# Kernel tuning notes

Measured on AMD Instinct MI355X. Metric: run time of the kernel, lower is better.

## Reference

```python
import jax, jax.numpy as jnp
import numpy as np

NUM_BUCKETS = 32
MAX_DISTANCE = 128
N_HEADS = 16
D_KV = 64


def relative_position_bucket(rel, num_buckets=NUM_BUCKETS, max_distance=MAX_DISTANCE):
    # bidirectional (encoder) bucketing, matches the torch reference
    nb = num_buckets // 2
    ret = (rel > 0).astype(jnp.int32) * nb
    rp = jnp.abs(rel)
    max_exact = nb // 2
    is_small = rp < max_exact
    # guard log(0); masked out by is_small anyway
    large = max_exact + (
        jnp.log(jnp.maximum(rp, 1).astype(jnp.float32) / max_exact)
        / np.log(max_distance / max_exact)
        * (nb - max_exact)
    ).astype(jnp.int32)
    large = jnp.minimum(large, nb - 1)
    return ret + jnp.where(is_small, rp, large)


def compute_bias(rel_bias_table, q_len, k_len):
    q_pos = jnp.arange(q_len)[:, None]
    k_pos = jnp.arange(k_len)[None, :]
    buckets = relative_position_bucket(k_pos - q_pos)  # [S, K]
    bias = rel_bias_table[buckets]                      # [S, K, H]
    return jnp.transpose(bias, (2, 0, 1))[None]         # [1, H, S, K]


def setup_inputs() -> dict:
    key = jax.random.key(0)
    ks = jax.random.split(key, 6)
    d_model, inner = 1024, N_HEADS * D_KV
    scale = 1.0 / np.sqrt(d_model)
    return {
        "hidden_states": jax.random.normal(ks[0], (4, 2048, d_model), jnp.float32),
        "Wq": jax.random.normal(ks[1], (d_model, inner), jnp.float32) * scale,
        "Wk": jax.random.normal(ks[2], (d_model, inner), jnp.float32) * scale,
        "Wv": jax.random.normal(ks[3], (d_model, inner), jnp.float32) * scale,
        "Wo": jax.random.normal(ks[4], (inner, d_model), jnp.float32) * scale,
        "rel_bias_table": jax.random.normal(ks[5], (NUM_BUCKETS, N_HEADS), jnp.float32),
    }


def reference(hidden_states, Wq, Wk, Wv, Wo, rel_bias_table):
    B, S, _ = hidden_states.shape
    K_len = S  # self-attention (key_value_states is None)
    q = (hidden_states @ Wq).reshape(B, S, N_HEADS, D_KV)
    k = (hidden_states @ Wk).reshape(B, K_len, N_HEADS, D_KV)
    v = (hidden_states @ Wv).reshape(B, K_len, N_HEADS, D_KV)
    # NOTE: T5 attention has no 1/sqrt(d_kv) scaling
    scores = jnp.einsum("bshd,bkhd->bhsk", q, k)
    pos_bias = compute_bias(rel_bias_table, S, K_len)
    attn = jax.nn.softmax(scores + pos_bias, axis=-1)
    out = jnp.einsum("bhsk,bkhd->bshd", attn, v).reshape(B, S, N_HEADS * D_KV)
    out = out @ Wo
    return (out, pos_bias)
```

## Files before the change

### kernel.cpp

```cpp
#include <hip/hip_runtime.h>
#include <cstdint>
#include <cstddef>

typedef unsigned short u16;
typedef unsigned int u32;
typedef __attribute__((ext_vector_type(8))) short bf16x8;
typedef __attribute__((ext_vector_type(4))) float f32x4;
typedef __attribute__((ext_vector_type(16))) float f32x16;
typedef __attribute__((ext_vector_type(2))) unsigned int u32x2;

#define MFMA(a, b, c)   __builtin_amdgcn_mfma_f32_16x16x32_bf16((a), (b), (c), 0, 0, 0)
#define MFMA32(a, b, c) __builtin_amdgcn_mfma_f32_32x32x16_bf16((a), (b), (c), 0, 0, 0)

typedef const __attribute__((address_space(1))) void gv1_t;
typedef __attribute__((address_space(3))) void lv3_t;
#define GLOAD_LDS16(g, l) __builtin_amdgcn_global_load_lds((gv1_t*)(g), (lv3_t*)(l), 16, 0, 0)

#define BATCH 4
#define SEQ 2048
#define DMODEL 1024
#define NHEAD 16
#define MROWS (BATCH * SEQ)
#define QKVN (3 * DMODEL)

#define LOG2E 1.44269504088896340736f

__device__ __forceinline__ u16 f2bf(float f) {
  u32 x = __builtin_bit_cast(u32, f);
  x += 0x7fffu + ((x >> 16) & 1u);
  return (u16)(x >> 16);
}

__device__ __forceinline__ u32 pkbf(float a, float b) {
  return (u32)f2bf(a) | ((u32)f2bf(b) << 16);
}

__device__ __forceinline__ u32x2 plswap(u32 a, u32 b) {
  return __builtin_amdgcn_permlane32_swap(a, b, false, false);
}

extern "C" __device__ float __ocml_exp2_f32(float);
__device__ __forceinline__ float exp2fast(float x) {
#if __has_builtin(__builtin_amdgcn_exp2f)
  return __builtin_amdgcn_exp2f(x);
#else
  return __ocml_exp2_f32(x);
#endif
}

__global__ __launch_bounds__(256) void convert_h(const float* __restrict__ H,
                                                 u16* __restrict__ Hb) {
  size_t i = (size_t)blockIdx.x * 1024 + threadIdx.x * 4;
  float4 v = *(const float4*)&H[i];
  uint2 o;
  o.x = pkbf(v.x, v.y);
  o.y = pkbf(v.z, v.w);
  *(uint2*)&Hb[i] = o;
}

__global__ void transpose_w(const float* __restrict__ Wq, const float* __restrict__ Wk,
                            const float* __restrict__ Wv, const float* __restrict__ Wo,
                            u16* __restrict__ Wt) {
  __shared__ u16 Ts[32][33];
  const float* W = (blockIdx.z == 0) ? Wq : (blockIdx.z == 1) ? Wk
                   : (blockIdx.z == 2) ? Wv : Wo;
  const float s = (blockIdx.z == 0) ? LOG2E : 1.0f;
  int x = threadIdx.x, y0 = threadIdx.y;
  int r0 = blockIdx.y * 32, c0 = blockIdx.x * 32;
  for (int yy = y0; yy < 32; yy += 8)
    Ts[yy][x] = f2bf(W[(size_t)(r0 + yy) * 1024 + c0 + x] * s);
  __syncthreads();
  for (int yy = y0; yy < 32; yy += 8)
    Wt[(size_t)(blockIdx.z * 1024 + c0 + yy) * 1024 + r0 + x] = Ts[x][yy];
}

__device__ __forceinline__ int rel_bucket(int rel) {
  int ret = (rel > 0) ? 16 : 0;
  int rp = (rel < 0) ? -rel : rel;
  if (rp < 8) return ret + rp;
  int i = 0;
  i += (rp >= 12); i += (rp >= 16); i += (rp >= 23); i += (rp >= 32);
  i += (rp >= 46); i += (rp >= 64); i += (rp >= 91);
  return ret + 8 + i;
}

__global__ __launch_bounds__(256) void build_bias_rel(const float* __restrict__ tbl,
                                                      float* __restrict__ brel,
                                                      float* __restrict__ brel2) {
  int h = blockIdx.x;
  for (int rix = threadIdx.x; rix < 4095; rix += 256) {
    float v = tbl[rel_bucket(rix - 2047) * NHEAD + h];
    brel[h * 4096 + rix] = v;
    brel2[h * 4096 + rix] = v * LOG2E;
  }
}

__global__ __launch_bounds__(256) void gemm_bf16k(const u16* __restrict__ A,
                                                  const u16* __restrict__ Bt,
                                                  u16* __restrict__ Cb, float* __restrict__ Cf,
                                                  int M, int N, int K) {
  __shared__ u16 As[128 * 32];
  __shared__ u16 Bs[128 * 32];
  const int t = threadIdx.x;
  const int w = t >> 6, lane = t & 63, quad = lane >> 4, l15 = lane & 15;
  const int wr = w >> 1, wc = w & 1;

  const int nwg = gridDim.x * gridDim.y;
  const int orig = blockIdx.y * gridDim.x + blockIdx.x;
  const int wg = (orig & 7) * (nwg >> 3) + (orig >> 3);
  const int bx = wg % gridDim.x, by = wg / gridDim.x;
  const int row0 = by * 128, col0 = bx * 128;

  f32x4 acc[4][4];
  #pragma unroll
  for (int i = 0; i < 4; ++i)
    #pragma unroll
    for (int j = 0; j < 4; ++j) acc[i][j] = (f32x4){0.f, 0.f, 0.f, 0.f};

  const int srow = lane >> 2, scol = (lane & 3) * 8;

  for (int k0 = 0; k0 < K; k0 += 32) {
    #pragma unroll
    for (int p = 0; p < 2; ++p) {
      const int rb = w * 32 + p * 16;
      GLOAD_LDS16(&A[(size_t)(row0 + rb + srow) * K + k0 + scol], &As[rb * 32]);
      GLOAD_LDS16(&Bt[(size_t)(col0 + rb + srow) * K + k0 + scol], &Bs[rb * 32]);
    }
    __syncthreads();
    bf16x8 af[4], bfr[4];
    #pragma unroll
    for (int i = 0; i < 4; ++i)
      af[i] = *(const bf16x8*)&As[(wr * 64 + i * 16 + l15) * 32 + quad * 8];
    #pragma unroll
    for (int j = 0; j < 4; ++j)
      bfr[j] = *(const bf16x8*)&Bs[(wc * 64 + j * 16 + l15) * 32 + quad * 8];
    #pragma unroll
    for (int i = 0; i < 4; ++i)
      #pragma unroll
      for (int j = 0; j < 4; ++j)
        acc[i][j] = MFMA(af[i], bfr[j], acc[i][j]);
    __syncthreads();
  }
  #pragma unroll
  for (int i = 0; i < 4; ++i) {
    #pragma unroll
    for (int j = 0; j < 4; ++j) {
      int col = col0 + wc * 64 + j * 16 + l15;
      #pragma unroll
      for (int r = 0; r < 4; ++r) {
        int row = row0 + wr * 64 + i * 16 + quad * 4 + r;
        if (Cb) Cb[(size_t)row * N + col] = f2bf(acc[i][j][r]);
        else    Cf[(size_t)row * N + col] = acc[i][j][r];
      }
    }
  }
}

__global__ __launch_bounds__(256) void transpose_v(const u16* __restrict__ QKV,
                                                   u16* __restrict__ Vt) {
  __shared__ u16 Ts[64 * 72];
  int st = blockIdx.x, bh = blockIdx.y;
  int b = bh >> 4, h = bh & 15;
  int t = threadIdx.x;
  #pragma unroll
  for (int p = 0; p < 2; ++p) {
    int c = t * 2 + p, r = c >> 3, cc = (c & 7) * 8;
    *(uint4*)&Ts[r * 72 + cc] =
        *(const uint4*)&QKV[(size_t)(b * SEQ + st * 64 + r) * QKVN + 2 * DMODEL + h * 64 + cc];
  }
  __syncthreads();
  #pragma unroll
  for (int p = 0; p < 2; ++p) {
    int c = t * 2 + p, d = c >> 3, s8 = (c & 7) * 8;
    union { u16 u[8]; uint4 v; } tmp;
    #pragma unroll
    for (int jj = 0; jj < 8; ++jj) tmp.u[jj] = Ts[(s8 + jj) * 72 + d];
    *(uint4*)&Vt[((size_t)(bh * 64 + d)) * SEQ + st * 64 + s8] = tmp.v;
  }
}

__global__ __launch_bounds__(256) void attn_fused(const u16* __restrict__ QKV,
                                                  const u16* __restrict__ Vt,
                                                  const float* __restrict__ brel,
                                                  const float* __restrict__ brel2,
                                                  u16* __restrict__ Aout,
                                                  float* __restrict__ pb) {
  __shared__ u16 Ks[64 * 72];
  __shared__ u16 Vs[64 * 72];
  const int qt = blockIdx.x, bh = blockIdx.y;
  const int b = bh >> 4, h = bh & 15;
  const int t = threadIdx.x;
  const int w = t >> 6, lane = t & 63, l31 = lane & 31, h5 = lane >> 5;
  const int qb = qt * 128;
  const int qw0 = qb + w * 32;
  const int qr = qw0 + l31;
  const bool wrbias = (bh < 16);

  const float cpos = brel2[h * 4096 + 4040];
  const float cneg = brel2[h * 4096 + 54];
  const float cpu  = brel[h * 4096 + 4040];
  const float cnu  = brel[h * 4096 + 54];

  const u16* qptr = QKV + (size_t)(b * SEQ + qr) * QKVN + h * 64 + h5 * 8;
  bf16x8 qf[4];
  #pragma unroll
  for (int ks = 0; ks < 4; ++ks) qf[ks] = *(const bf16x8*)(qptr + ks * 16);

  float lsum = 0.f;
  f32x16 oacc[2];
  #pragma unroll
  for (int m = 0; m < 2; ++m)
    #pragma unroll
    for (int i = 0; i < 16; ++i) oacc[m][i] = 0.f;

  const int c0 = t * 2, c1 = c0 + 1;
  const int r0s = c0 >> 3, cc0 = (c0 & 7) * 8;
  const int r1s = c1 >> 3, cc1 = (c1 & 7) * 8;
  const size_t krow = (size_t)(b * SEQ) * QKVN + DMODEL + h * 64;
  const size_t vtrow = (size_t)bh * 64;
  const float* brow = brel2 + h * 4096 + 2047;

  uint4 ka0 = *(const uint4*)&QKV[krow + (size_t)r0s * QKVN + cc0];
  uint4 ka1 = *(const uint4*)&QKV[krow + (size_t)r1s * QKVN + cc1];
  uint4 va0 = *(const uint4*)&Vt[(vtrow + r0s) * SEQ + cc0];
  uint4 va1 = *(const uint4*)&Vt[(vtrow + r1s) * SEQ + cc1];

  for (int kb = 0; kb < SEQ; kb += 64) {
    *(uint4*)&Ks[r0s * 72 + cc0] = ka0;
    *(uint4*)&Ks[r1s * 72 + cc1] = ka1;
    *(uint4*)&Vs[r0s * 72 + cc0] = va0;
    *(uint4*)&Vs[r1s * 72 + cc1] = va1;
    __syncthreads();

    if (kb + 64 < SEQ) {
      ka0 = *(const uint4*)&QKV[krow + (size_t)(kb + 64 + r0s) * QKVN + cc0];
      ka1 = *(const uint4*)&QKV[krow + (size_t)(kb + 64 + r1s) * QKVN + cc1];
      va0 = *(const uint4*)&Vt[(vtrow + r0s) * SEQ + kb + 64 + cc0];
      va1 = *(const uint4*)&Vt[(vtrow + r1s) * SEQ + kb + 64 + cc1];
    }

    f32x16 sc[2];
    __builtin_amdgcn_s_setprio(1);
    #pragma unroll
    for (int m = 0; m < 2; ++m) {
      #pragma unroll
      for (int i = 0; i < 16; ++i) sc[m][i] = 0.f;
      #pragma unroll
      for (int ks = 0; ks < 4; ++ks) {
        bf16x8 kf = *(const bf16x8*)&Ks[(m * 32 + l31) * 72 + ks * 16 + h5 * 8];
        sc[m] = MFMA32(kf, qf[ks], sc[m]);
      }
    }
    __builtin_amdgcn_s_setprio(0);

    if (wrbias) {
      const int pr = qb + (t >> 1);
      const int pc = kb + (t & 1) * 32;
      float* po = pb + ((size_t)(h * SEQ + pr)) * SEQ + pc;
      const int lo = pc - pr;
      if (lo >= 91 || lo + 31 <= -91) {
        const float c = (lo >= 91) ? cpu : cnu;
        const float4 vv = {c, c, c, c};
        #pragma unroll
        for (int i = 0; i < 8; ++i) *(float4*)&po[i * 4] = vv;
      } else {
        const float* bb = brel + h * 4096 + 2047 - pr + pc;
        #pragma unroll
        for (int i = 0; i < 8; ++i) {
          float4 vv;
          vv.x = bb[i * 4]; vv.y = bb[i * 4 + 1];
          vv.z = bb[i * 4 + 2]; vv.w = bb[i * 4 + 3];
          *(float4*)&po[i * 4] = vv;
        }
      }
    }

    bf16x8 bp[4];
    #pragma unroll
    for (int m = 0; m < 2; ++m) {
      const int kb32 = kb + 32 * m;
      if (kb32 >= qw0 + 122) {
        #pragma unroll
        for (int i = 0; i < 16; ++i) sc[m][i] += cpos;
      } else if (kb32 <= qw0 - 122) {
        #pragma unroll
        for (int i = 0; i < 16; ++i) sc[m][i] += cneg;
      } else {
        const float* bb = brow + kb32 + 4 * h5 - qr;
        #pragma unroll
        for (int i = 0; i < 16; ++i) sc[m][i] += bb[(i & 3) + 8 * (i >> 2)];
      }
      u32 w0[4], w1[4];
      #pragma unroll
      for (int tt = 0; tt < 4; ++tt) {
        float p0 = exp2fast(sc[m][4 * tt + 0]);
        float p1 = exp2fast(sc[m][4 * tt + 1]);
        float p2 = exp2fast(sc[m][4 * tt + 2]);
        float p3 = exp2fast(sc[m][4 * tt + 3]);
        lsum += (p0 + p1) + (p2 + p3);
        w0[tt] = pkbf(p0, p1);
        w1[tt] = pkbf(p2, p3);
      }
      u32x2 r0 = plswap(w0[0], w0[1]);
      u32x2 r1 = plswap(w1[0], w1[1]);
      u32x2 r2 = plswap(w0[2], w0[3]);
      u32x2 r3 = plswap(w1[2], w1[3]);
      union { u32 u[4]; bf16x8 v; } q0, q1;
      q0.u[0] = r0.x; q0.u[1] = r1.x; q0.u[2] = r0.y; q0.u[3] = r1.y;
      q1.u[0] = r2.x; q1.u[1] = r3.x; q1.u[2] = r2.y; q1.u[3] = r3.y;
      bp[2 * m]     = q0.v;
      bp[2 * m + 1] = q1.v;
    }

    __builtin_amdgcn_s_setprio(1);
    #pragma unroll
    for (int m2 = 0; m2 < 2; ++m2)
      #pragma unroll
      for (int ks = 0; ks < 4; ++ks) {
        bf16x8 vf = *(const bf16x8*)&Vs[(m2 * 32 + l31) * 72 + ks * 16 + h5 * 8];
        oacc[m2] = MFMA32(vf, bp[ks], oacc[m2]);
      }
    __builtin_amdgcn_s_setprio(0);
    __syncthreads();
  }

  lsum += __shfl_xor(lsum, 32);
  const float inv = 1.0f / lsum;
  const size_t rowb = (size_t)(b * SEQ + qr) * DMODEL + h * 64;
  #pragma unroll
  for (int m2 = 0; m2 < 2; ++m2)
    #pragma unroll
    for (int tt = 0; tt < 4; ++tt) {
      uint2 o;
      o.x = pkbf(oacc[m2][4 * tt + 0] * inv, oacc[m2][4 * tt + 1] * inv);
      o.y = pkbf(oacc[m2][4 * tt + 2] * inv, oacc[m2][4 * tt + 3] * inv);
      *(uint2*)&Aout[rowb + 32 * m2 + 8 * tt + 4 * h5] = o;
    }
}

extern "C" void kernel_launch(void* const* d_in, const int* in_sizes, int n_in,
                              void* d_out, int out_size, void* d_ws, size_t ws_size,
                              hipStream_t stream) {
  (void)in_sizes; (void)n_in; (void)out_size; (void)ws_size;
  const float* H   = (const float*)d_in[0];
  const float* Wq  = (const float*)d_in[1];
  const float* Wk  = (const float*)d_in[2];
  const float* Wv  = (const float*)d_in[3];
  const float* Wo  = (const float*)d_in[4];
  const float* tbl = (const float*)d_in[5];

  float* out = (float*)d_out;
  float* pos_bias = out + (size_t)MROWS * DMODEL;

  char* ws = (char*)d_ws;
  u16* Hb     = (u16*)(ws);
  u16* Wt     = (u16*)(ws + 16777216);
  u16* QKV    = (u16*)(ws + 25165824);
  u16* Vt     = (u16*)(ws + 75497472);
  float* brel  = (float*)(ws + 92274688);
  float* brel2 = (float*)(ws + 92536832);

  convert_h<<<8192, 256, 0, stream>>>(H, Hb);
  transpose_w<<<dim3(32, 32, 4), dim3(32, 8), 0, stream>>>(Wq, Wk, Wv, Wo, Wt);
  build_bias_rel<<<16, 256, 0, stream>>>(tbl, brel, brel2);

  gemm_bf16k<<<dim3(QKVN / 128, MROWS / 128), 256, 0, stream>>>(
      Hb, Wt, QKV, nullptr, MROWS, QKVN, DMODEL);
  transpose_v<<<dim3(32, 64), 256, 0, stream>>>(QKV, Vt);
  attn_fused<<<dim3(16, 64), 256, 0, stream>>>(QKV, Vt, brel, brel2,
                                               Hb , pos_bias);
  gemm_bf16k<<<dim3(DMODEL / 128, MROWS / 128), 256, 0, stream>>>(
      Hb, Wt + (size_t)QKVN * DMODEL, nullptr, out, MROWS, DMODEL, DMODEL);
}
```

Measured before the change: 596.9 us.

## Double-buffer K/V tiles in LDS and spread bias writes across batches

```diff
diff --git a/kernel.cpp b/kernel.cpp
--- a/kernel.cpp
+++ b/kernel.cpp
@@ -185,8 +185,8 @@
                                                   const float* __restrict__ brel2,
                                                   u16* __restrict__ Aout,
                                                   float* __restrict__ pb) {
-  __shared__ u16 Ks[64 * 72];
-  __shared__ u16 Vs[64 * 72];
+  __shared__ u16 Ks[2][64 * 72];
+  __shared__ u16 Vs[2][64 * 72];
   const int qt = blockIdx.x, bh = blockIdx.y;
   const int b = bh >> 4, h = bh & 15;
   const int t = threadIdx.x;
@@ -194,7 +194,6 @@
   const int qb = qt * 128;
   const int qw0 = qb + w * 32;
   const int qr = qw0 + l31;
-  const bool wrbias = (bh < 16);
 
   const float cpos = brel2[h * 4096 + 4040];
   const float cneg = brel2[h * 4096 + 54];
@@ -224,15 +223,20 @@
   uint4 ka1 = *(const uint4*)&QKV[krow + (size_t)r1s * QKVN + cc1];
   uint4 va0 = *(const uint4*)&Vt[(vtrow + r0s) * SEQ + cc0];
   uint4 va1 = *(const uint4*)&Vt[(vtrow + r1s) * SEQ + cc1];
-
-  for (int kb = 0; kb < SEQ; kb += 64) {
-    *(uint4*)&Ks[r0s * 72 + cc0] = ka0;
-    *(uint4*)&Ks[r1s * 72 + cc1] = ka1;
-    *(uint4*)&Vs[r0s * 72 + cc0] = va0;
-    *(uint4*)&Vs[r1s * 72 + cc1] = va1;
-    __syncthreads();
-
-    if (kb + 64 < SEQ) {
+  *(uint4*)&Ks[0][r0s * 72 + cc0] = ka0;
+  *(uint4*)&Ks[0][r1s * 72 + cc1] = ka1;
+  *(uint4*)&Vs[0][r0s * 72 + cc0] = va0;
+  *(uint4*)&Vs[0][r1s * 72 + cc1] = va1;
+  __syncthreads();
+
+  #pragma unroll 2
+  for (int ti = 0; ti < SEQ / 64; ++ti) {
+    const int kb = ti * 64;
+    const int cur = ti & 1;
+    const u16* Kc = Ks[cur];
+    const u16* Vc = Vs[cur];
+
+    if (ti + 1 < SEQ / 64) {
       ka0 = *(const uint4*)&QKV[krow + (size_t)(kb + 64 + r0s) * QKVN + cc0];
       ka1 = *(const uint4*)&QKV[krow + (size_t)(kb + 64 + r1s) * QKVN + cc1];
       va0 = *(const uint4*)&Vt[(vtrow + r0s) * SEQ + kb + 64 + cc0];
@@ -247,13 +251,13 @@
       for (int i = 0; i < 16; ++i) sc[m][i] = 0.f;
       #pragma unroll
       for (int ks = 0; ks < 4; ++ks) {
-        bf16x8 kf = *(const bf16x8*)&Ks[(m * 32 + l31) * 72 + ks * 16 + h5 * 8];
+        bf16x8 kf = *(const bf16x8*)&Kc[(m * 32 + l31) * 72 + ks * 16 + h5 * 8];
         sc[m] = MFMA32(kf, qf[ks], sc[m]);
       }
     }
     __builtin_amdgcn_s_setprio(0);
 
-    if (wrbias) {
+    if ((ti & 3) == b) {
       const int pr = qb + (t >> 1);
       const int pc = kb + (t & 1) * 32;
       float* po = pb + ((size_t)(h * SEQ + pr)) * SEQ + pc;
@@ -317,10 +321,19 @@
     for (int m2 = 0; m2 < 2; ++m2)
       #pragma unroll
       for (int ks = 0; ks < 4; ++ks) {
-        bf16x8 vf = *(const bf16x8*)&Vs[(m2 * 32 + l31) * 72 + ks * 16 + h5 * 8];
+        bf16x8 vf = *(const bf16x8*)&Vc[(m2 * 32 + l31) * 72 + ks * 16 + h5 * 8];
         oacc[m2] = MFMA32(vf, bp[ks], oacc[m2]);
       }
     __builtin_amdgcn_s_setprio(0);
+
+    if (ti + 1 < SEQ / 64) {
+      u16* Kn = Ks[cur ^ 1];
+      u16* Vn = Vs[cur ^ 1];
+      *(uint4*)&Kn[r0s * 72 + cc0] = ka0;
+      *(uint4*)&Kn[r1s * 72 + cc1] = ka1;
+      *(uint4*)&Vn[r0s * 72 + cc0] = va0;
+      *(uint4*)&Vn[r1s * 72 + cc1] = va1;
+    }
     __syncthreads();
   }
 
```

Result: no change. 586.6 us (-1.7%).
